# Performance work log

Hardware: AMD Instinct MI355X
Metric: run time of the kernel (lower is better)

Reference implementation:

```python
import jax, jax.numpy as jnp
import numpy as np
import math

B, S, D, H = 4, 2048, 1024, 16
HD = D // H  # 64

def setup_inputs() -> dict:
    key = jax.random.key(0)
    ks = jax.random.split(key, 4)
    x = jax.random.normal(ks[0], (B, S, D), dtype=jnp.float32)
    # causal mask, True = attend (precomputed as in the original usage)
    mask = jnp.tril(jnp.ones((S, S), dtype=bool))[None, None, :, :]
    c_attn_w = jax.random.normal(ks[1], (D, 3 * D), dtype=jnp.float32) * 0.02
    c_attn_b = jnp.zeros((3 * D,), dtype=jnp.float32)
    c_proj_w = jax.random.normal(ks[2], (D, D), dtype=jnp.float32) * 0.02
    c_proj_b = jnp.zeros((D,), dtype=jnp.float32)
    return {"x": x, "mask": mask, "c_attn_w": c_attn_w, "c_attn_b": c_attn_b,
            "c_proj_w": c_proj_w, "c_proj_b": c_proj_b}

def reference(x, mask, c_attn_w, c_attn_b, c_proj_w, c_proj_b):
    b, s, d = x.shape
    # c_attn: Conv1D acts as Linear with transposed weight convention
    qkv = x @ c_attn_w + c_attn_b                      # [B,S,3D]
    q, k, v = jnp.split(qkv, 3, axis=-1)
    q = q.reshape(b, s, H, HD).transpose(0, 2, 1, 3)   # [B,H,S,hd]
    k = k.reshape(b, s, H, HD).transpose(0, 2, 1, 3)   # [B,H,S,hd]
    v = v.reshape(b, s, H, HD).transpose(0, 2, 1, 3)   # [B,H,S,hd]
    # scores, scale by sqrt(head_dim) (done unconditionally in _attn)
    w = jnp.einsum('bhqd,bhkd->bhqk', q, k) / math.sqrt(HD)
    # masked_fill_(1 - mask, -10000.0)
    w = jnp.where(mask, w, jnp.float32(-10000.0))
    w = jax.nn.softmax(w, axis=-1)                     # attn_dropout p=0
    a = jnp.einsum('bhqk,bhkd->bhqd', w, v)            # [B,H,S,hd]
    a = a.transpose(0, 2, 1, 3).reshape(b, s, d)       # merge heads
    out = a @ c_proj_w + c_proj_b                      # resid_dropout p=0
    return out
```

## Files before the change

kernel.cpp:

```cpp
#include <hip/hip_runtime.h>

#define SEQ  2048
#define DIM  1024
#define NH   16
#define HD   64
#define NB   4

typedef __bf16 bf16_t;
typedef bf16_t bf16x8 __attribute__((ext_vector_type(8)));
typedef bf16_t bf16x4 __attribute__((ext_vector_type(4)));
typedef float  floatx4 __attribute__((ext_vector_type(4)));

#define MFMA16(a, b, c) __builtin_amdgcn_mfma_f32_16x16x32_bf16((a), (b), (c), 0, 0, 0)

__device__ __forceinline__ void gl_lds16(const bf16_t* g, bf16_t* l) {
    __builtin_amdgcn_global_load_lds(
        (const __attribute__((address_space(1))) void*)g,
        (__attribute__((address_space(3))) void*)l,
        16, 0, 0);
}

#define VM4 asm volatile("s_waitcnt vmcnt(4)" ::: "memory")
#define VM0 asm volatile("s_waitcnt vmcnt(0)" ::: "memory")
#define NOPS ((void)0)

__global__ __launch_bounds__(256) void prep(
    const float* __restrict__ x, bf16_t* __restrict__ xb,
    const float* __restrict__ wqkv, bf16_t* __restrict__ wqkvT,
    const float* __restrict__ wproj, bf16_t* __restrict__ wprojT) {
    const int bid = blockIdx.x, tid = threadIdx.x;
    if (bid < 8192) {
        const int i = (bid * 256 + tid) * 4;
        const float4 v = *(const float4*)(x + i);
        xb[i + 0] = (bf16_t)v.x;
        xb[i + 1] = (bf16_t)v.y;
        xb[i + 2] = (bf16_t)v.z;
        xb[i + 3] = (bf16_t)v.w;
        return;
    }
    __shared__ bf16_t t[32][33];
    const float* in;
    bf16_t* out;
    int R, C, bx, by;
    if (bid < 8192 + 3072) {
        const int idx = bid - 8192;
        in = wqkv; out = wqkvT; R = 1024; C = 3072;
        bx = idx % 96; by = idx / 96;
    } else {
        const int idx = bid - 11264;
        in = wproj; out = wprojT; R = 1024; C = 1024;
        bx = idx & 31; by = idx >> 5;
    }
    const int c0 = bx * 32, r0 = by * 32;
    const int tx = tid & 31, ty = tid >> 5;
#pragma unroll
    for (int i = 0; i < 32; i += 8)
        t[ty + i][tx] = (bf16_t)in[(r0 + ty + i) * C + c0 + tx];
    __syncthreads();
#pragma unroll
    for (int i = 0; i < 32; i += 8)
        out[(c0 + ty + i) * R + r0 + tx] = t[tx][ty + i];
}

__global__ __launch_bounds__(512, 2) void gemm256_qkv(
    const bf16_t* __restrict__ A, const bf16_t* __restrict__ Bt,
    const float* __restrict__ bias, int K,
    bf16_t* __restrict__ Qo, bf16_t* __restrict__ Ko, bf16_t* __restrict__ Vo) {
    __shared__ __align__(16) bf16_t smem[65536];
    bf16_t* As = smem;
    bf16_t* Bs = smem + 32768;

    const int bid = blockIdx.x;
    const int swz = (bid & 7) * 48 + (bid >> 3);
    const int m0 = (swz / 12) * 256, n0 = (swz % 12) * 256;

    const int tid = threadIdx.x;
    const int w = tid >> 6, lane = tid & 63;
    const int l15 = lane & 15, quad = lane >> 4;
    const int wr = w >> 2, wc = w & 3;
    const int xk = l15 & 7;

    floatx4 acc[8][4] = {};

    const int strow = tid >> 3;
    const int stg = ((tid & 7) - strow) & 7;
    const bf16_t* aA = A + (size_t)(m0 + strow) * K + stg * 8;
    const bf16_t* aB = Bt + (size_t)(n0 + strow) * K + stg * 8;

    auto stA = [&](int buf, int kt, int h) {
        const bf16_t* p = aA + ((size_t)h * 128) * K + kt * 64;
        bf16_t* d = As + buf * 16384 + h * 8192 + tid * 8;
        gl_lds16(p, d);
        gl_lds16(p + (size_t)64 * K, d + 4096);
    };
    auto stB = [&](int buf, int kt, int h) {
        const bf16_t* p = aB + ((size_t)h * 128) * K + kt * 64;
        bf16_t* d = Bs + buf * 16384 + h * 8192 + tid * 8;
        gl_lds16(p, d);
        gl_lds16(p + (size_t)64 * K, d + 4096);
    };

    const bf16_t* Awave0 = As + wr * 8192;
    const bf16_t* Bwave0 = Bs + (wc >> 1) * 8192 + (wc & 1) * 4096;

    bf16x8 bfr[4][2];

#define PHASE(BUF, Q, STAGE, VMW)                                              \
    do {                                                                       \
        const bf16_t* Ab_ = Awave0 + (BUF) * 16384;                            \
        const bf16_t* Bb_ = Bwave0 + (BUF) * 16384;                            \
        if ((Q) == 0) {                                                        \
            _Pragma("unroll") for (int j_ = 0; j_ < 4; j_++)                   \
                _Pragma("unroll") for (int kk_ = 0; kk_ < 2; kk_++)            \
                    bfr[j_][kk_] = *(const bf16x8*)&Bb_[(j_ * 16 + l15) * 64 + \
                        (((kk_ * 4 + quad) + xk) & 7) * 8];                    \
        }                                                                      \
        bf16x8 af_[2][2];                                                      \
        _Pragma("unroll") for (int di_ = 0; di_ < 2; di_++)                    \
            _Pragma("unroll") for (int kk_ = 0; kk_ < 2; kk_++)                \
                af_[di_][kk_] = *(const bf16x8*)&Ab_[(((Q) * 2 + di_) * 16 + l15) * 64 + \
                    (((kk_ * 4 + quad) + xk) & 7) * 8];                        \
        STAGE;                                                                 \
        VMW;                                                                   \
        asm volatile("" ::: "memory");                                         \
        __builtin_amdgcn_s_barrier();                                          \
        asm volatile("s_waitcnt lgkmcnt(0)" ::: "memory");                     \
        __builtin_amdgcn_s_setprio(1);                                         \
        _Pragma("unroll") for (int di_ = 0; di_ < 2; di_++)                    \
            _Pragma("unroll") for (int j_ = 0; j_ < 4; j_++) {                 \
                acc[(Q) * 2 + di_][j_] =                                       \
                    MFMA16(bfr[j_][0], af_[di_][0], acc[(Q) * 2 + di_][j_]);   \
                acc[(Q) * 2 + di_][j_] =                                       \
                    MFMA16(bfr[j_][1], af_[di_][1], acc[(Q) * 2 + di_][j_]);   \
            }                                                                  \
        __builtin_amdgcn_s_setprio(0);                                         \
        asm volatile("" ::: "memory");                                         \
        __builtin_amdgcn_s_barrier();                                          \
        asm volatile("" ::: "memory");                                         \
    } while (0)

    const int NT = K >> 6;
    const int NI = NT >> 1;

    stA(0, 0, 0); stA(0, 0, 1); stB(0, 0, 0); stB(0, 0, 1);
    stB(1, 1, 0); stB(1, 1, 1);
    VM4;
    asm volatile("" ::: "memory");
    __builtin_amdgcn_s_barrier();
    asm volatile("" ::: "memory");

    for (int it = 0; it < NI - 1; ++it) {
        const int T1 = 2 * it + 1, T2 = 2 * it + 2, T3 = 2 * it + 3;
        PHASE(0, 0, stA(1, T1, 0), NOPS);
        PHASE(0, 1, stA(1, T1, 1), NOPS);
        PHASE(0, 2, stB(0, T2, 0), NOPS);
        PHASE(0, 3, stB(0, T2, 1), VM4);
        PHASE(1, 0, stA(0, T2, 0), NOPS);
        PHASE(1, 1, stA(0, T2, 1), NOPS);
        PHASE(1, 2, stB(1, T3, 0), NOPS);
        PHASE(1, 3, stB(1, T3, 1), VM4);
    }
    {
        PHASE(0, 0, stA(1, NT - 1, 0), NOPS);
        PHASE(0, 1, stA(1, NT - 1, 1), NOPS);
        PHASE(0, 2, NOPS, NOPS);
        PHASE(0, 3, NOPS, VM0);
        PHASE(1, 0, NOPS, NOPS);
        PHASE(1, 1, NOPS, NOPS);
        PHASE(1, 2, NOPS, NOPS);
        PHASE(1, 3, NOPS, NOPS);
    }
#undef PHASE

    bf16_t* Et = smem;
    const int which = n0 >> 10;
    const float qs = (which == 0) ? 0.18033688f : 1.0f;
#pragma unroll
    for (int c = 0; c < 2; ++c) {
        if (c) __syncthreads();
        if (wr == c) {
#pragma unroll
            for (int j = 0; j < 4; j++) {
                const int nc = wc * 64 + j * 16 + quad * 4;
#pragma unroll
                for (int i = 0; i < 8; i++) {
                    const int mrow = i * 16 + l15;
                    bf16x4 pk;
#pragma unroll
                    for (int r = 0; r < 4; r++)
                        pk[r] = (bf16_t)((acc[i][j][r] + bias[n0 + nc + r]) * qs);
                    *(bf16x4*)&Et[mrow * 264 + nc] = pk;
                }
            }
        }
        __syncthreads();
        if (which < 2) {
            const int row = tid >> 2, seg = tid & 3;
            const int m = m0 + c * 128 + row, b = m >> 11, s = m & 2047;
            const int h = ((n0 & 1023) >> 6) + seg;
            bf16_t* dst = (which == 0 ? Qo : Ko) + ((size_t)(b * NH + h) * SEQ + s) * HD;
            const bf16_t* src = Et + row * 264 + seg * 64;
#pragma unroll
            for (int g = 0; g < 8; g++)
                *(bf16x8*)(dst + g * 8) = *(const bf16x8*)(src + g * 8);
        } else {
            const int line = tid >> 1, sh = (tid & 1) << 6;
            const int seg = line >> 6, d = line & 63;
            const int h = ((n0 & 1023) >> 6) + seg;
            const int b = m0 >> 11;
            const int sbase = (m0 & 2047) + c * 128 + sh;
            bf16_t* dst = Vo + ((size_t)(b * NH + h) * HD + d) * SEQ + sbase;
#pragma unroll
            for (int g = 0; g < 8; g++) {
                bf16x8 tv;
#pragma unroll
                for (int e = 0; e < 8; e++)
                    tv[e] = Et[(sh + g * 8 + e) * 264 + seg * 64 + d];
                *(bf16x8*)(dst + g * 8) = tv;
            }
        }
    }
}

template <int MODE>
__global__ __launch_bounds__(256, 2) void gemm128(
    const bf16_t* __restrict__ A, const bf16_t* __restrict__ Bt,
    const float* __restrict__ bias, int K, float* __restrict__ Co) {
    __shared__ __align__(16) bf16_t smem[128 * 128];
    bf16_t* Al = smem;
    bf16_t* Bl = smem + 128 * 64;

    const int tid = threadIdx.x;
    const int m0 = blockIdx.y * 128, n0 = blockIdx.x * 128;
    const int w = tid >> 6, lane = tid & 63;
    const int l15 = lane & 15, quad = lane >> 4;
    const int wm = (w & 1) * 64, wn = (w >> 1) * 64;

    floatx4 acc[4][4] = {};

    const int g_st = ((tid & 7) - (tid >> 3)) & 7;
    const bf16_t* aptr = A + (m0 + (tid >> 3)) * K + g_st * 8;
    const bf16_t* bptr = Bt + (n0 + (tid >> 3)) * K + g_st * 8;
    bf16_t* al = Al + tid * 8;
    bf16_t* bl = Bl + tid * 8;

    for (int k0 = 0; k0 < K; k0 += 64) {
#pragma unroll
        for (int c = 0; c < 4; c++) {
            gl_lds16(aptr + (c * 32) * K, al + c * 2048);
            gl_lds16(bptr + (c * 32) * K, bl + c * 2048);
        }
        aptr += 64;
        bptr += 64;
        __syncthreads();

#pragma unroll
        for (int h = 0; h < 2; h++) {
            const int sAB = (((h << 2) + quad + (l15 & 7)) & 7) * 8;
            bf16x8 af[4], bfr[4];
#pragma unroll
            for (int i = 0; i < 4; i++)
                af[i] = *(const bf16x8*)&Al[(wm + i * 16 + l15) * 64 + sAB];
#pragma unroll
            for (int j = 0; j < 4; j++)
                bfr[j] = *(const bf16x8*)&Bl[(wn + j * 16 + l15) * 64 + sAB];
#pragma unroll
            for (int i = 0; i < 4; i++)
#pragma unroll
                for (int j = 0; j < 4; j++)
                    acc[i][j] = MFMA16(af[i], bfr[j], acc[i][j]);
        }
        __syncthreads();
    }

#pragma unroll
    for (int j = 0; j < 4; j++) {
        const int n = n0 + wn + j * 16 + l15;
        const float bv = bias[n];
#pragma unroll
        for (int i = 0; i < 4; i++)
#pragma unroll
            for (int r = 0; r < 4; r++) {
                const int m = m0 + wm + i * 16 + quad * 4 + r;
                Co[m * 1024 + n] = acc[i][j][r] + bv;
            }
    }
}

__global__ __launch_bounds__(256, 3) void attn1q(
    const bf16_t* __restrict__ Q, const bf16_t* __restrict__ Kg,
    const bf16_t* __restrict__ Vt, bf16_t* __restrict__ Aout) {
    __shared__ __align__(16) bf16_t Ks[2 * 64 * 64];
    __shared__ __align__(16) bf16_t Vs[2 * 64 * 64];
    __shared__ __align__(16) bf16_t Ps[128 * 64];

    const int bh = blockIdx.x;
    const int qt = 15 - blockIdx.y;
    const int nk = 2 * qt + 2;

    const int tid = threadIdx.x, w = tid >> 6, lane = tid & 63;
    const int l15 = lane & 15, quad = lane >> 4;
    const int b = bh >> 4, hd = bh & 15;
    const int xk = l15 & 7;

    bf16x8 aq[2][2];
#pragma unroll
    for (int i = 0; i < 2; i++) {
        const bf16_t* qr = Q + (size_t)(bh * SEQ + qt * 128 + w * 32 + i * 16 + l15) * HD;
#pragma unroll
        for (int h = 0; h < 2; h++)
            aq[i][h] = *(const bf16x8*)(qr + h * 32 + quad * 8);
    }

    floatx4 o[2][4] = {};
    float li[2] = {};

    const int srow = tid >> 3;
    const int sg = (tid & 7) ^ (srow & 7);
    const bf16_t* kgl = Kg + (size_t)bh * SEQ * HD + (size_t)srow * HD + sg * 8;
    const bf16_t* vgl = Vt + (size_t)bh * HD * SEQ + (size_t)srow * SEQ + sg * 8;

    auto stage = [&](int buf, int kt) {
        const bf16_t* kp = kgl + kt * (64 * HD);
        const bf16_t* vp = vgl + kt * 64;
        bf16_t* kd = Ks + buf * 4096 + tid * 8;
        bf16_t* vd = Vs + buf * 4096 + tid * 8;
        gl_lds16(kp, kd);
        gl_lds16(kp + 32 * HD, kd + 2048);
        gl_lds16(vp, vd);
        gl_lds16(vp + 32 * SEQ, vd + 2048);
    };

    auto proc = [&](int kt, int buf) {
        const bf16_t* Ksub = Ks + buf * 4096;
        const bf16_t* Vsub = Vs + buf * 4096;
        bf16x8 bk[4][2];
#pragma unroll
        for (int j = 0; j < 4; j++) {
            const int n = j * 16 + l15;
#pragma unroll
            for (int h = 0; h < 2; h++)
                bk[j][h] = *(const bf16x8*)&Ksub[n * 64 + (((h * 4 + quad) ^ xk) * 8)];
        }
        floatx4 z[2][4] = {};
        __builtin_amdgcn_s_setprio(1);
#pragma unroll
        for (int i = 0; i < 2; i++)
#pragma unroll
            for (int j = 0; j < 4; j++) {
                z[i][j] = MFMA16(bk[j][0], aq[i][0], z[i][j]);
                z[i][j] = MFMA16(bk[j][1], aq[i][1], z[i][j]);
            }
        __builtin_amdgcn_s_setprio(0);
#pragma unroll
        for (int i = 0; i < 2; i++) {
            const int qbase = qt * 128 + w * 32 + i * 16;
            const int qrow_l = qbase + l15;
            const bool full = (kt * 64 + 63) <= qbase;
            const int prow = w * 32 + i * 16 + l15;
            bf16_t* pbase = Ps + prow * 64;
            const int rx = prow & 7;
#pragma unroll
            for (int j = 0; j < 4; j++) {
                const int kg0 = kt * 64 + j * 16 + quad * 4;
                bf16x4 pk;
                float es[4];
#pragma unroll
                for (int r = 0; r < 4; r++) {
                    float e = __builtin_amdgcn_exp2f(z[i][j][r]);
                    if (!full && kg0 + r > qrow_l) e = 0.f;
                    es[r] = e;
                    pk[r] = (bf16_t)e;
                }
                li[i] += (es[0] + es[1]) + (es[2] + es[3]);
                const int g = 2 * j + (quad >> 1);
                *(bf16x4*)(pbase + (((g ^ rx) << 3) | ((quad & 1) << 2))) = pk;
            }
        }
        __builtin_amdgcn_s_waitcnt(0xC07F);
        bf16x8 ap[2][2];
#pragma unroll
        for (int i = 0; i < 2; i++) {
            const int row = w * 32 + i * 16 + l15;
#pragma unroll
            for (int kk = 0; kk < 2; kk++)
                ap[i][kk] = *(const bf16x8*)&Ps[row * 64 +
                                               (((kk * 4 + quad) ^ (row & 7)) << 3)];
        }
        bf16x8 bv[4][2];
#pragma unroll
        for (int j = 0; j < 4; j++) {
            const int n = j * 16 + l15;
#pragma unroll
            for (int kk = 0; kk < 2; kk++)
                bv[j][kk] = *(const bf16x8*)&Vsub[n * 64 + (((kk * 4 + quad) ^ xk) * 8)];
        }
        __builtin_amdgcn_s_setprio(1);
#pragma unroll
        for (int i = 0; i < 2; i++)
#pragma unroll
            for (int j = 0; j < 4; j++) {
                o[i][j] = MFMA16(ap[i][0], bv[j][0], o[i][j]);
                o[i][j] = MFMA16(ap[i][1], bv[j][1], o[i][j]);
            }
        __builtin_amdgcn_s_setprio(0);
    };

    stage(0, 0);
    __syncthreads();
    for (int kt = 0; kt < nk; ++kt) {
        const int cur = kt & 1;
        if (kt + 1 < nk) stage(cur ^ 1, kt + 1);
        proc(kt, cur);
        __syncthreads();
    }

#pragma unroll
    for (int i = 0; i < 2; i++) {
        float s = li[i];
        s += __shfl_xor(s, 16, 64);
        s += __shfl_xor(s, 32, 64);
#pragma unroll
        for (int r = 0; r < 4; r++) {
            const float sv = __shfl(s, quad * 4 + r, 64);
            const float inv = 1.0f / sv;
            const int srow_o = qt * 128 + w * 32 + i * 16 + quad * 4 + r;
            bf16_t* orow = Aout + (size_t)(b * SEQ + srow_o) * DIM + hd * HD;
#pragma unroll
            for (int j = 0; j < 4; j++)
                orow[j * 16 + l15] = (bf16_t)(o[i][j][r] * inv);
        }
    }
}

extern "C" void kernel_launch(void* const* d_in, const int* in_sizes, int n_in,
                              void* d_out, int out_size, void* d_ws, size_t ws_size,
                              hipStream_t stream) {
    const float* x        = (const float*)d_in[0];
    const float* c_attn_w = (const float*)d_in[2];
    const float* c_attn_b = (const float*)d_in[3];
    const float* c_proj_w = (const float*)d_in[4];
    const float* c_proj_b = (const float*)d_in[5];
    float* out = (float*)d_out;

    char* ws = (char*)d_ws;
    bf16_t* xb     = (bf16_t*)ws; ws += (size_t)NB * SEQ * DIM * 2;
    bf16_t* wqkvT  = (bf16_t*)ws; ws += (size_t)3072 * 1024 * 2;
    bf16_t* wprojT = (bf16_t*)ws; ws += (size_t)1024 * 1024 * 2;
    bf16_t* Qb  = (bf16_t*)ws; ws += (size_t)NB * NH * SEQ * HD * 2;
    bf16_t* Kb  = (bf16_t*)ws; ws += (size_t)NB * NH * SEQ * HD * 2;
    bf16_t* Vtb = (bf16_t*)ws; ws += (size_t)NB * NH * SEQ * HD * 2;
    bf16_t* Ab  = (bf16_t*)ws; ws += (size_t)NB * SEQ * DIM * 2;

    prep<<<12288, 256, 0, stream>>>(x, xb, c_attn_w, wqkvT, c_proj_w, wprojT);

    gemm256_qkv<<<384, 512, 0, stream>>>(xb, wqkvT, c_attn_b, 1024,
                                         Qb, Kb, Vtb);

    attn1q<<<dim3(NB * NH, 16), 256, 0, stream>>>(Qb, Kb, Vtb, Ab);

    gemm128<1><<<dim3(8, 64), 256, 0, stream>>>(Ab, wprojT, c_proj_b, 1024, out);
}
```

Baseline: 259.1 us.

## Restructure QKV GEMM into quadrant phases with finer-grained load pipeline

The 256x256 QKV GEMM now splits each k-tile into four quadrant phases. Each wave computes a 64x32 sub-tile per quadrant instead of owning a fixed 128x64 strip, and A/B fragments are reused across quadrant pairs. The global-to-LDS staging schedule is reordered into a one-tile-per-iteration loop with vmcnt waits moved after the MFMA block, aiming to overlap loads better. It also adds sched_barrier and rewrites the epilogue so every wave writes in both halves. The projection GEMM template is renamed without behaviour change.

```diff
diff --git a/kernel.cpp b/kernel.cpp
--- a/kernel.cpp
+++ b/kernel.cpp
@@ -20,6 +20,8 @@
         16, 0, 0);
 }
 
+#define VM8 asm volatile("s_waitcnt vmcnt(8)" ::: "memory")
+#define VM6 asm volatile("s_waitcnt vmcnt(6)" ::: "memory")
 #define VM4 asm volatile("s_waitcnt vmcnt(4)" ::: "memory")
 #define VM0 asm volatile("s_waitcnt vmcnt(0)" ::: "memory")
 #define NOPS ((void)0)
@@ -77,10 +79,10 @@
     const int tid = threadIdx.x;
     const int w = tid >> 6, lane = tid & 63;
     const int l15 = lane & 15, quad = lane >> 4;
-    const int wr = w >> 2, wc = w & 3;
+    const int swr = w >> 2, swc = w & 3;
     const int xk = l15 & 7;
 
-    floatx4 acc[8][4] = {};
+    floatx4 acc[2][2][4][2] = {};
 
     const int strow = tid >> 3;
     const int stg = ((tid & 7) - strow) & 7;
@@ -100,77 +102,74 @@
         gl_lds16(p + (size_t)64 * K, d + 4096);
     };
 
-    const bf16_t* Awave0 = As + wr * 8192;
-    const bf16_t* Bwave0 = Bs + (wc >> 1) * 8192 + (wc & 1) * 4096;
-
-    bf16x8 bfr[4][2];
-
-#define PHASE(BUF, Q, STAGE, VMW)                                              \
+    bf16x8 afr[4][2];
+    bf16x8 bfr[2][2];
+
+#define PH(BUF, QM, QN, RA, STAGE, VMW)                                        \
     do {                                                                       \
-        const bf16_t* Ab_ = Awave0 + (BUF) * 16384;                            \
-        const bf16_t* Bb_ = Bwave0 + (BUF) * 16384;                            \
-        if ((Q) == 0) {                                                        \
-            _Pragma("unroll") for (int j_ = 0; j_ < 4; j_++)                   \
+        const bf16_t* Ah_ = As + (BUF) * 16384 + (QM) * 8192;                  \
+        const bf16_t* Bh_ = Bs + (BUF) * 16384 + (QN) * 8192;                  \
+        if (RA) {                                                              \
+            _Pragma("unroll") for (int mi_ = 0; mi_ < 4; mi_++)                \
                 _Pragma("unroll") for (int kk_ = 0; kk_ < 2; kk_++)            \
-                    bfr[j_][kk_] = *(const bf16x8*)&Bb_[(j_ * 16 + l15) * 64 + \
+                    afr[mi_][kk_] = *(const bf16x8*)&Ah_[                      \
+                        (swr * 64 + mi_ * 16 + l15) * 64 +                     \
                         (((kk_ * 4 + quad) + xk) & 7) * 8];                    \
         }                                                                      \
-        bf16x8 af_[2][2];                                                      \
-        _Pragma("unroll") for (int di_ = 0; di_ < 2; di_++)                    \
+        _Pragma("unroll") for (int nj_ = 0; nj_ < 2; nj_++)                    \
             _Pragma("unroll") for (int kk_ = 0; kk_ < 2; kk_++)                \
-                af_[di_][kk_] = *(const bf16x8*)&Ab_[(((Q) * 2 + di_) * 16 + l15) * 64 + \
+                bfr[nj_][kk_] = *(const bf16x8*)&Bh_[                          \
+                    (swc * 32 + nj_ * 16 + l15) * 64 +                         \
                     (((kk_ * 4 + quad) + xk) & 7) * 8];                        \
         STAGE;                                                                 \
-        VMW;                                                                   \
         asm volatile("" ::: "memory");                                         \
         __builtin_amdgcn_s_barrier();                                          \
         asm volatile("s_waitcnt lgkmcnt(0)" ::: "memory");                     \
+        __builtin_amdgcn_sched_barrier(0);                                     \
         __builtin_amdgcn_s_setprio(1);                                         \
-        _Pragma("unroll") for (int di_ = 0; di_ < 2; di_++)                    \
-            _Pragma("unroll") for (int j_ = 0; j_ < 4; j_++) {                 \
-                acc[(Q) * 2 + di_][j_] =                                       \
-                    MFMA16(bfr[j_][0], af_[di_][0], acc[(Q) * 2 + di_][j_]);   \
-                acc[(Q) * 2 + di_][j_] =                                       \
-                    MFMA16(bfr[j_][1], af_[di_][1], acc[(Q) * 2 + di_][j_]);   \
+        _Pragma("unroll") for (int mi_ = 0; mi_ < 4; mi_++)                    \
+            _Pragma("unroll") for (int nj_ = 0; nj_ < 2; nj_++) {              \
+                acc[QM][QN][mi_][nj_] =                                        \
+                    MFMA16(bfr[nj_][0], afr[mi_][0], acc[QM][QN][mi_][nj_]);   \
+                acc[QM][QN][mi_][nj_] =                                        \
+                    MFMA16(bfr[nj_][1], afr[mi_][1], acc[QM][QN][mi_][nj_]);   \
             }                                                                  \
         __builtin_amdgcn_s_setprio(0);                                         \
+        VMW;                                                                   \
         asm volatile("" ::: "memory");                                         \
         __builtin_amdgcn_s_barrier();                                          \
         asm volatile("" ::: "memory");                                         \
     } while (0)
 
     const int NT = K >> 6;
-    const int NI = NT >> 1;
-
-    stA(0, 0, 0); stA(0, 0, 1); stB(0, 0, 0); stB(0, 0, 1);
-    stB(1, 1, 0); stB(1, 1, 1);
-    VM4;
+
+    stA(0, 0, 0); stB(0, 0, 0); stA(0, 0, 1); stB(0, 0, 1);
+    stA(1, 1, 0); stB(1, 1, 0);
+    VM8;
     asm volatile("" ::: "memory");
     __builtin_amdgcn_s_barrier();
     asm volatile("" ::: "memory");
 
-    for (int it = 0; it < NI - 1; ++it) {
-        const int T1 = 2 * it + 1, T2 = 2 * it + 2, T3 = 2 * it + 3;
-        PHASE(0, 0, stA(1, T1, 0), NOPS);
-        PHASE(0, 1, stA(1, T1, 1), NOPS);
-        PHASE(0, 2, stB(0, T2, 0), NOPS);
-        PHASE(0, 3, stB(0, T2, 1), VM4);
-        PHASE(1, 0, stA(0, T2, 0), NOPS);
-        PHASE(1, 1, stA(0, T2, 1), NOPS);
-        PHASE(1, 2, stB(1, T3, 0), NOPS);
-        PHASE(1, 3, stB(1, T3, 1), VM4);
+    for (int s = 0; s < NT - 2; ++s) {
+        const int buf = s & 1;
+        PH(buf, 0, 0, 1, stA(buf ^ 1, s + 1, 1), VM6);
+        PH(buf, 0, 1, 0, stB(buf ^ 1, s + 1, 1), VM8);
+        PH(buf, 1, 0, 1, stA(buf, s + 2, 0), NOPS);
+        PH(buf, 1, 1, 0, stB(buf, s + 2, 0), VM8);
     }
     {
-        PHASE(0, 0, stA(1, NT - 1, 0), NOPS);
-        PHASE(0, 1, stA(1, NT - 1, 1), NOPS);
-        PHASE(0, 2, NOPS, NOPS);
-        PHASE(0, 3, NOPS, VM0);
-        PHASE(1, 0, NOPS, NOPS);
-        PHASE(1, 1, NOPS, NOPS);
-        PHASE(1, 2, NOPS, NOPS);
-        PHASE(1, 3, NOPS, NOPS);
-    }
-#undef PHASE
+        PH(0, 0, 0, 1, stA(1, NT - 1, 1), VM6);
+        PH(0, 0, 1, 0, stB(1, NT - 1, 1), VM8);
+        PH(0, 1, 0, 1, NOPS, NOPS);
+        PH(0, 1, 1, 0, NOPS, VM4);
+    }
+    {
+        PH(1, 0, 0, 1, NOPS, VM0);
+        PH(1, 0, 1, 0, NOPS, NOPS);
+        PH(1, 1, 0, 1, NOPS, NOPS);
+        PH(1, 1, 1, 0, NOPS, NOPS);
+    }
+#undef PH
 
     bf16_t* Et = smem;
     const int which = n0 >> 10;
@@ -178,21 +177,21 @@
 #pragma unroll
     for (int c = 0; c < 2; ++c) {
         if (c) __syncthreads();
-        if (wr == c) {
-#pragma unroll
-            for (int j = 0; j < 4; j++) {
-                const int nc = wc * 64 + j * 16 + quad * 4;
-#pragma unroll
-                for (int i = 0; i < 8; i++) {
-                    const int mrow = i * 16 + l15;
+#pragma unroll
+        for (int qn = 0; qn < 2; qn++)
+#pragma unroll
+            for (int nj = 0; nj < 2; nj++) {
+                const int nc = qn * 128 + swc * 32 + nj * 16 + quad * 4;
+#pragma unroll
+                for (int mi = 0; mi < 4; mi++) {
+                    const int mrow = swr * 64 + mi * 16 + l15;
                     bf16x4 pk;
 #pragma unroll
                     for (int r = 0; r < 4; r++)
-                        pk[r] = (bf16_t)((acc[i][j][r] + bias[n0 + nc + r]) * qs);
+                        pk[r] = (bf16_t)((acc[c][qn][mi][nj][r] + bias[n0 + nc + r]) * qs);
                     *(bf16x4*)&Et[mrow * 264 + nc] = pk;
                 }
             }
-        }
         __syncthreads();
         if (which < 2) {
             const int row = tid >> 2, seg = tid & 3;
@@ -222,8 +221,7 @@
     }
 }
 
-template <int MODE>
-__global__ __launch_bounds__(256, 2) void gemm128(
+__global__ __launch_bounds__(256, 2) void gemm128p(
     const bf16_t* __restrict__ A, const bf16_t* __restrict__ Bt,
     const float* __restrict__ bias, int K, float* __restrict__ Co) {
     __shared__ __align__(16) bf16_t smem[128 * 128];
@@ -459,5 +457,5 @@
 
     attn1q<<<dim3(NB * NH, 16), 256, 0, stream>>>(Qb, Kb, Vtb, Ab);
 
-    gemm128<1><<<dim3(8, 64), 256, 0, stream>>>(Ab, wprojT, c_proj_b, 1024, out);
-}
+    gemm128p<<<dim3(8, 64), 256, 0, stream>>>(Ab, wprojT, c_proj_b, 1024, out);
+}
```

Result: no change. 263.0 us (+1.5%).
